# Optimization experiments

Measured on AMD Instinct MI355X. Metric: run time of the kernel, lower is better.

Reference implementation:

```python
import jax, jax.numpy as jnp
import numpy as np

D_STATE = 11
DT_RANK = 4
BN_EPS = 1e-5
RMS_EPS = 1e-5


def setup_inputs() -> dict:
    key = jax.random.key(0)
    ks = jax.random.split(key, 8)
    B, L, D = 8, 8192, 64
    x = jax.random.normal(ks[0], (B, L, D), dtype=jnp.float32)
    tconv_w = jax.random.normal(ks[1], (64, 1, 63), dtype=jnp.float32) * 0.1
    bn_gamma = jnp.ones((64,), jnp.float32)
    bn_beta = jnp.zeros((64,), jnp.float32)
    x_proj_weight = jax.random.normal(ks[2], (1, DT_RANK + 2 * D_STATE, 64), jnp.float32) * (64 ** -0.5)
    dt_projs_weight = jax.random.uniform(ks[3], (1, 64, DT_RANK), jnp.float32, -0.5, 0.5)
    # dt bias ~ inverse-softplus of dt in [1e-3, 1e-1]
    dt = jnp.exp(jax.random.uniform(ks[4], (1, 64), jnp.float32) * (np.log(0.1) - np.log(0.001)) + np.log(0.001))
    dt_projs_bias = dt + jnp.log(-jnp.expm1(-dt))
    A_logs = jnp.log(jnp.broadcast_to(jnp.arange(1, D_STATE + 1, dtype=jnp.float32), (64, D_STATE)))
    Ds = jnp.ones((64,), jnp.float32)
    rms_scale = jnp.ones((1, 64), jnp.float32)
    return {"x": x, "tconv_w": tconv_w, "bn_gamma": bn_gamma, "bn_beta": bn_beta,
            "x_proj_weight": x_proj_weight, "dt_projs_weight": dt_projs_weight,
            "dt_projs_bias": dt_projs_bias, "A_logs": A_logs, "Ds": Ds,
            "rms_scale": rms_scale}


def _silu(v):
    return v * jax.nn.sigmoid(v)


def reference(x, tconv_w, bn_gamma, bn_beta, x_proj_weight, dt_projs_weight,
              dt_projs_bias, A_logs, Ds, rms_scale):
    B, L, D = x.shape  # D == 64
    z = x
    xc = jnp.transpose(x, (0, 2, 1))  # (B, C, L)

    # depthwise conv1d, kernel 63, pad 31, no bias
    xc = jax.lax.conv_general_dilated(
        xc, tconv_w, window_strides=(1,), padding=[(31, 31)],
        feature_group_count=D, dimension_numbers=("NCH", "OIH", "NCH"))

    # BatchNorm1d (training-mode forward: batch stats, biased variance)
    mean = jnp.mean(xc, axis=(0, 2), keepdims=True)
    var = jnp.mean((xc - mean) ** 2, axis=(0, 2), keepdims=True)
    xc = (xc - mean) / jnp.sqrt(var + BN_EPS) * bn_gamma[None, :, None] + bn_beta[None, :, None]

    u = _silu(xc)  # (B, d_inner, L)

    # x_proj: (B,d,L) x (C,d) -> (B,C,L)
    x_dbl = jnp.einsum("bdl,cd->bcl", u, x_proj_weight[0])
    dts = x_dbl[:, :DT_RANK]                      # (B, r, L)
    Bs = x_dbl[:, DT_RANK:DT_RANK + D_STATE]      # (B, N, L)
    Cs = x_dbl[:, DT_RANK + D_STATE:]             # (B, N, L)

    dts = jnp.einsum("brl,dr->bdl", dts, dt_projs_weight[0])
    delta = jax.nn.softplus(dts + dt_projs_bias[0][None, :, None])  # (B,d,L)

    A = -jnp.exp(A_logs)  # (d, N)
    dA = jnp.exp(jnp.einsum("bdl,dn->lbdn", delta, A))      # (L,B,d,N)
    dBu = jnp.einsum("bdl,bnl->lbdn", delta * u, Bs)        # (L,B,d,N)

    def step(h, inp):
        dA_t, dBu_t = inp
        h = dA_t * h + dBu_t
        return h, h

    h0 = jnp.zeros((B, u.shape[1], D_STATE), dtype=u.dtype)
    _, hs = jax.lax.scan(step, h0, (dA, dBu))  # (L,B,d,N)

    y = jnp.einsum("lbdn,bnl->bdl", hs, Cs) + Ds[None, :, None] * u  # (B,d,L)

    y = jnp.transpose(y, (0, 2, 1))  # (B, L, d_inner)

    # RMSNorm
    ms = jnp.mean(y ** 2, axis=-1, keepdims=True)
    y = (rms_scale / jnp.sqrt(ms + RMS_EPS)) * y

    out = y * _silu(z)
    return out
```

## Files before the change

### kernel.cpp

```cpp
#include <hip/hip_runtime.h>
#include <hip/hip_bf16.h>
#include <math.h>

#define NB 8
#define LL 8192
#define DD 64
#define NS 11
#define NR 4
#define NC 512
#define LC (LL/NC)
#define CONV_LT 64
#define KW 63
#define PJ 64
#define NBKT 16
#define US 68
#define WS 72

__device__ __forceinline__ float sigmoidf_(float v){ return 1.f/(1.f+__expf(-v)); }

__global__ void k_zero(float* __restrict__ p){
  p[blockIdx.x*256 + threadIdx.x] = 0.f;
}

__global__ __launch_bounds__(256,4) void k_conv(const float* __restrict__ x,
                                              const float* __restrict__ w,
                                              float* __restrict__ xc,
                                              float* __restrict__ bn_acc){
  const int b  = blockIdx.x / (LL/CONV_LT);
  const int lt = blockIdx.x % (LL/CONV_LT);
  const int l0 = lt*CONV_LT;
  __shared__ float xt[(CONV_LT+62)*DD];
  __shared__ float rs[256], rq[256];
  const int t = threadIdx.x;
  for (int i=t; i<(CONV_LT+62)*DD; i+=256){
    int lrel = i/DD, d = i%DD;
    int lg = l0 - 31 + lrel;
    xt[i] = (lg>=0 && lg<LL) ? x[((size_t)b*LL+lg)*DD + d] : 0.f;
  }
  __syncthreads();
  const int d = t & 63;
  const int base = (t >> 6) * 16;
  float acc[16];
  #pragma unroll
  for (int j=0;j<16;j++) acc[j]=0.f;
  #pragma unroll 1
  for (int kb=0; kb<4; ++kb){
    float wv[16];
    #pragma unroll
    for (int kk=0;kk<16;kk++){
      int k = kb*16+kk;
      wv[kk] = (k<KW) ? w[d*KW+k] : 0.f;
    }
    float xw[31];
    #pragma unroll
    for (int i=0;i<31;i++) xw[i] = xt[(base+kb*16+i)*DD + d];
    #pragma unroll
    for (int j=0;j<16;j++){
      #pragma unroll
      for (int kk=0;kk<16;kk++){
        acc[j] = fmaf(wv[kk], xw[j+kk], acc[j]);
      }
    }
  }
  float lsum=0.f, lsq=0.f;
  #pragma unroll
  for (int j=0;j<16;j++){
    xc[((size_t)b*LL + l0+base+j)*DD + d] = acc[j];
    lsum += acc[j]; lsq = fmaf(acc[j],acc[j],lsq);
  }
  rs[t]=lsum; rq[t]=lsq;
  __syncthreads();
  if (t<64){
    float s = rs[t]+rs[t+64]+rs[t+128]+rs[t+192];
    float q = rq[t]+rq[t+64]+rq[t+128]+rq[t+192];
    const int bkt = (blockIdx.x & (NBKT-1))*128;
    atomicAdd(&bn_acc[bkt+t],    s);
    atomicAdd(&bn_acc[bkt+64+t], q);
  }
}

__global__ __launch_bounds__(256,4) void k_proj(const float* __restrict__ xc,
                                              const float* __restrict__ bn_acc,
                                              const float* __restrict__ gamma,
                                              const float* __restrict__ beta,
                                              const float* __restrict__ xpw,
                                              const float* __restrict__ dtw,
                                              const float* __restrict__ dtb,
                                              const float* __restrict__ Alog,
                                              float* __restrict__ duo,
                                              float* __restrict__ bc,
                                              float* __restrict__ chunkst){
  const int b  = blockIdx.x / (LL/PJ);
  const int lt = blockIdx.x % (LL/PJ);
  const int l0 = lt*PJ;
  __shared__ float ul[PJ*US];
  __shared__ float bcl[PJ][24];
  __shared__ float wsh2[26*WS];
  __shared__ float xd[PJ*NR];
  __shared__ float dtwsh[64*NR];
  const int t = threadIdx.x;
  for (int i=t; i<26*64; i+=256){ int c=i>>6, dd=i&63; wsh2[c*WS+dd] = xpw[i]; }
  dtwsh[t] = dtw[t];
  const int d = t & 63, wv = t >> 6;
  float msum = 0.f, qsum = 0.f;
  #pragma unroll
  for (int k=0;k<NBKT;k++){
    msum += bn_acc[k*128 + d];
    qsum += bn_acc[k*128 + 64 + d];
  }
  const float inv_n = 1.f/((float)NB*(float)LL);
  float mean = msum*inv_n;
  float var  = qsum*inv_n - mean*mean;
  float sc = gamma[d] * rsqrtf(var + 1e-5f);
  float sh = beta[d] - mean*sc;
  float uu[16];
  #pragma unroll
  for (int j=0;j<16;j++){
    int lr = wv*16 + j;
    float v = xc[((size_t)b*LL + l0+lr)*DD + d];
    v = fmaf(v, sc, sh);
    float u_ = v * sigmoidf_(v);
    uu[j] = u_;
    ul[lr*US+d] = u_;
  }
  __syncthreads();
  {
    const int cp  = t & 15;
    const int lrb = t >> 4;
    if (cp < 13){
      float acc0[4] = {0.f,0.f,0.f,0.f};
      float acc1[4] = {0.f,0.f,0.f,0.f};
      #pragma unroll 2
      for (int dd4=0; dd4<16; ++dd4){
        float4 w0 = *reinterpret_cast<const float4*>(&wsh2[(2*cp  )*WS + dd4*4]);
        float4 w1 = *reinterpret_cast<const float4*>(&wsh2[(2*cp+1)*WS + dd4*4]);
        #pragma unroll
        for (int p=0;p<4;p++){
          float4 uv = *reinterpret_cast<const float4*>(&ul[(lrb*4+p)*US + dd4*4]);
          acc0[p] = fmaf(w0.x,uv.x, fmaf(w0.y,uv.y, fmaf(w0.z,uv.z, fmaf(w0.w,uv.w, acc0[p]))));
          acc1[p] = fmaf(w1.x,uv.x, fmaf(w1.y,uv.y, fmaf(w1.z,uv.z, fmaf(w1.w,uv.w, acc1[p]))));
        }
      }
      #pragma unroll
      for (int cc=0; cc<2; ++cc){
        int c = 2*cp+cc;
        #pragma unroll
        for (int p=0;p<4;p++){
          int lr = lrb*4+p;
          float v = cc ? acc1[p] : acc0[p];
          if (c < NR) xd[lr*NR+c] = v;
          else {
            int pos = c - NR;
            int slot = (pos < NS) ? pos : pos+1;
            bcl[lr][slot] = v;
            bc[((size_t)b*LL + l0+lr)*24 + slot] = v;
          }
        }
      }
    }
  }
  __syncthreads();
  {
    const float bias = dtb[d];
    const float dw0 = dtwsh[d*NR+0], dw1 = dtwsh[d*NR+1],
                dw2 = dtwsh[d*NR+2], dw3 = dtwsh[d*NR+3];
    float a0 = -__expf(Alog[d*NS]);
    bool fast = true;
    #pragma unroll
    for (int n=1;n<NS;n++){
      float an = -__expf(Alog[d*NS+n]);
      fast = fast && (fabsf(an - (float)(n+1)*a0) <= 1e-4f*(float)(n+1));
    }
    const int task = b*NC + lt*4 + wv;
    float h[12];
    #pragma unroll
    for (int n=0;n<12;n++) h[n]=0.f;
    float dsum=0.f;
    #pragma unroll 4
    for (int l=0;l<LC;++l){
      int lr = wv*LC + l;
      float4 xv = *reinterpret_cast<const float4*>(&xd[lr*NR]);
      float s = fmaf(dw0,xv.x, fmaf(dw1,xv.y, fmaf(dw2,xv.z, fmaf(dw3,xv.w, bias))));
      float de = fmaxf(s,0.f) + __logf(1.f + __expf(-fabsf(s)));
      float u_ = uu[l];
      float du = de*u_;
      dsum += de;
      float2 st; st.x = de; st.y = u_;
      *reinterpret_cast<float2*>(duo + (((size_t)b*LL + l0+lr)*DD + d)*2) = st;
      float bca[12];
      const float4* q = reinterpret_cast<const float4*>(&bcl[lr][0]);
      *reinterpret_cast<float4*>(&bca[0]) = q[0];
      *reinterpret_cast<float4*>(&bca[4]) = q[1];
      *reinterpret_cast<float4*>(&bca[8]) = q[2];
      if (fast){
        float r = __expf(a0*de);
        float dA = 1.f;
        #pragma unroll
        for (int n=0;n<NS;n++){
          dA *= r;
          h[n] = fmaf(dA, h[n], du*bca[n]);
        }
      } else {
        #pragma unroll
        for (int n=0;n<NS;n++){
          float dA = __expf(-__expf(Alog[d*NS+n])*de);
          h[n] = fmaf(dA, h[n], du*bca[n]);
        }
      }
    }
    h[11] = dsum;
    float4* o = reinterpret_cast<float4*>(chunkst + ((size_t)task*64 + d)*12);
    o[0] = *reinterpret_cast<float4*>(&h[0]);
    o[1] = *reinterpret_cast<float4*>(&h[4]);
    o[2] = *reinterpret_cast<float4*>(&h[8]);
  }
}

__global__ __launch_bounds__(64) void k_scanMid(const float* __restrict__ chunkst,
                                                const float* __restrict__ Alog,
                                                float* __restrict__ hin){
  const int wid  = blockIdx.x;
  const int lane = threadIdx.x & 63;
  const int b = wid >> 6, d = wid & 63;
  const int c0 = lane*8;
  const size_t recbase = (((size_t)b*NC + c0)*64 + d)*12;
  float aAll[NS];
  #pragma unroll
  for (int n=0;n<NS;n++) aAll[n] = -expf(Alog[d*NS+n]);
  bool fast = true;
  #pragma unroll
  for (int n=1;n<NS;n++)
    fast = fast && (fabsf(aAll[n] - (float)(n+1)*aAll[0]) <= 1e-4f*(float)(n+1));
  float Aa[NS], Bb[NS];
  #pragma unroll
  for (int n=0;n<NS;n++){ Aa[n]=1.f; Bb[n]=0.f; }
  #pragma unroll
  for (int j=0;j<8;j++){
    float rec[12];
    const float4* q = reinterpret_cast<const float4*>(chunkst + recbase + (size_t)j*768);
    *reinterpret_cast<float4*>(&rec[0]) = q[0];
    *reinterpret_cast<float4*>(&rec[4]) = q[1];
    *reinterpret_cast<float4*>(&rec[8]) = q[2];
    float ds = rec[11];
    if (fast){
      float r = __expf(aAll[0]*ds);
      float dA = 1.f;
      #pragma unroll
      for (int n=0;n<NS;n++){
        dA *= r;
        Bb[n] = fmaf(dA, Bb[n], rec[n]);
        Aa[n] *= dA;
      }
    } else {
      #pragma unroll
      for (int n=0;n<NS;n++){
        float dA = __expf(aAll[n]*ds);
        Bb[n] = fmaf(dA, Bb[n], rec[n]);
        Aa[n] *= dA;
      }
    }
  }
  #pragma unroll
  for (int n=0;n<NS;n++){
    float A = Aa[n], Bv = Bb[n];
    #pragma unroll
    for (int off=1; off<64; off<<=1){
      float Ap=__shfl_up(A,off,64), Bp=__shfl_up(Bv,off,64);
      if (lane>=off){ Bv = fmaf(A,Bp,Bv); A*=Ap; }
    }
    float hs = __shfl_up(Bv,1,64);
    Bb[n] = (lane==0) ? 0.f : hs;
  }
  #pragma unroll
  for (int j=0;j<8;j++){
    float rec[12];
    const float4* q = reinterpret_cast<const float4*>(chunkst + recbase + (size_t)j*768);
    *reinterpret_cast<float4*>(&rec[0]) = q[0];
    *reinterpret_cast<float4*>(&rec[4]) = q[1];
    *reinterpret_cast<float4*>(&rec[8]) = q[2];
    float ds = rec[11];
    float outv[12];
    if (fast){
      float r = __expf(aAll[0]*ds);
      float dA = 1.f;
      #pragma unroll
      for (int n=0;n<NS;n++){
        outv[n] = Bb[n];
        dA *= r;
        Bb[n] = fmaf(dA, Bb[n], rec[n]);
      }
    } else {
      #pragma unroll
      for (int n=0;n<NS;n++){
        outv[n] = Bb[n];
        float dA = __expf(aAll[n]*ds);
        Bb[n] = fmaf(dA, Bb[n], rec[n]);
      }
    }
    outv[11] = 0.f;
    float4* o = reinterpret_cast<float4*>(hin + recbase + (size_t)j*768);
    o[0] = *reinterpret_cast<float4*>(&outv[0]);
    o[1] = *reinterpret_cast<float4*>(&outv[4]);
    o[2] = *reinterpret_cast<float4*>(&outv[8]);
  }
}

__global__ __launch_bounds__(256,4) void k_scanB(const float* __restrict__ duo,
                                               const float* __restrict__ bc,
                                               const float* __restrict__ Alog,
                                               const float* __restrict__ hin,
                                               const float* __restrict__ Dsv,
                                               const float* __restrict__ rmss,
                                               const float* __restrict__ x,
                                               float* __restrict__ out){
  const int task = blockIdx.x*4 + (threadIdx.x>>6);
  const int d = threadIdx.x & 63;
  const int b = task / NC, c = task % NC;
  float a[NS], h[12];
  #pragma unroll
  for (int n=0;n<NS;n++) a[n] = -expf(Alog[d*NS+n]);
  bool fast = true;
  #pragma unroll
  for (int n=1;n<NS;n++)
    fast = fast && (fabsf(a[n] - (float)(n+1)*a[0]) <= 1e-4f*(float)(n+1));
  {
    const float4* q = reinterpret_cast<const float4*>(hin + ((size_t)task*64 + d)*12);
    *reinterpret_cast<float4*>(&h[0]) = q[0];
    *reinterpret_cast<float4*>(&h[4]) = q[1];
    *reinterpret_cast<float4*>(&h[8]) = q[2];
  }
  const float Dd = Dsv[d];
  const float rsc = rmss[d];
  const int l0 = c*LC;
  #pragma unroll 2
  for (int l=l0; l<l0+LC; ++l){
    size_t p = (size_t)b*LL + l;
    float2 du2 = *reinterpret_cast<const float2*>(duo + (p*DD+d)*2);
    float de = du2.x, uu = du2.y;
    float du = de*uu;
    float bca[24];
    const float4* q = reinterpret_cast<const float4*>(bc + p*24);
    *reinterpret_cast<float4*>(&bca[0])  = q[0];
    *reinterpret_cast<float4*>(&bca[4])  = q[1];
    *reinterpret_cast<float4*>(&bca[8])  = q[2];
    *reinterpret_cast<float4*>(&bca[12]) = q[3];
    *reinterpret_cast<float4*>(&bca[16]) = q[4];
    *reinterpret_cast<float4*>(&bca[20]) = q[5];
    float y = Dd*uu;
    if (fast){
      float r = __expf(a[0]*de);
      float dA = 1.f;
      #pragma unroll
      for (int n=0;n<NS;n++){
        dA *= r;
        h[n] = fmaf(dA, h[n], du*bca[n]);
        y = fmaf(h[n], bca[12+n], y);
      }
    } else {
      #pragma unroll
      for (int n=0;n<NS;n++){
        float dA = __expf(a[n]*de);
        h[n] = fmaf(dA, h[n], du*bca[n]);
        y = fmaf(h[n], bca[12+n], y);
      }
    }
    float ss = y*y;
    #pragma unroll
    for (int m=1;m<64;m<<=1) ss += __shfl_xor(ss, m, 64);
    float yn = rsc * rsqrtf(ss*(1.f/64.f) + 1e-5f) * y;
    float z = x[p*DD+d];
    out[p*DD+d] = yn * (z * sigmoidf_(z));
  }
}

extern "C" void kernel_launch(void* const* d_in, const int* in_sizes, int n_in,
                              void* d_out, int out_size, void* d_ws, size_t ws_size,
                              hipStream_t stream) {
  const float* x     = (const float*)d_in[0];
  const float* w     = (const float*)d_in[1];
  const float* gamma = (const float*)d_in[2];
  const float* beta  = (const float*)d_in[3];
  const float* xpw   = (const float*)d_in[4];
  const float* dtw   = (const float*)d_in[5];
  const float* dtb   = (const float*)d_in[6];
  const float* Alog  = (const float*)d_in[7];
  const float* Dsv   = (const float*)d_in[8];
  const float* rmss  = (const float*)d_in[9];
  float* out = (float*)d_out;

  float* f = (float*)d_ws;
  const size_t n_xld = (size_t)NB*LL*DD;
  float* xc      = f;
  float* duo     = xc + n_xld;
  float* bc      = duo + 2*n_xld;
  float* chunkst = bc + (size_t)NB*LL*24;
  float* hin     = chunkst + (size_t)NB*NC*64*12;
  float* bn_acc  = hin + (size_t)NB*NC*64*12;

  k_zero   <<<NBKT*128/256, 256, 0, stream>>>(bn_acc);
  k_conv   <<<NB*(LL/CONV_LT), 256, 0, stream>>>(x, w, xc, bn_acc);
  k_proj   <<<NB*(LL/PJ), 256, 0, stream>>>(xc, bn_acc, gamma, beta, xpw, dtw, dtb, Alog, duo, bc, chunkst);
  k_scanMid<<<NB*DD, 64, 0, stream>>>(chunkst, Alog, hin);
  k_scanB  <<<(NB*NC)/4, 256, 0, stream>>>(duo, bc, Alog, hin, Dsv, rmss, x, out);
}
```

Baseline: 95.10 us.

## Enlarge conv tiles, spread BN buckets, pack delta/u pairs as float4

The conv kernel now uses 128-row tiles with 512 threads, so fewer halo rows are reloaded per output row. BatchNorm partial sums are spread over 64 atomic buckets to reduce contention, and k_proj reduces those buckets in parallel across its four waves. The delta/u intermediate is stored two timesteps at a time as float4, so the scan kernel does wider loads. The scan kernel also drops its per-lane A array to save registers and recomputes exponentials on the slow path instead.

```diff
diff --git a/kernel.cpp b/kernel.cpp
--- a/kernel.cpp
+++ b/kernel.cpp
@@ -9,10 +9,10 @@
 #define NR 4
 #define NC 512
 #define LC (LL/NC)
-#define CONV_LT 64
+#define CONV_LT 128
 #define KW 63
 #define PJ 64
-#define NBKT 16
+#define NBKT 64
 #define US 68
 #define WS 72
 
@@ -22,7 +22,7 @@
   p[blockIdx.x*256 + threadIdx.x] = 0.f;
 }
 
-__global__ __launch_bounds__(256,4) void k_conv(const float* __restrict__ x,
+__global__ __launch_bounds__(512,4) void k_conv(const float* __restrict__ x,
                                               const float* __restrict__ w,
                                               float* __restrict__ xc,
                                               float* __restrict__ bn_acc){
@@ -30,9 +30,9 @@
   const int lt = blockIdx.x % (LL/CONV_LT);
   const int l0 = lt*CONV_LT;
   __shared__ float xt[(CONV_LT+62)*DD];
-  __shared__ float rs[256], rq[256];
+  __shared__ float rs[512], rq[512];
   const int t = threadIdx.x;
-  for (int i=t; i<(CONV_LT+62)*DD; i+=256){
+  for (int i=t; i<(CONV_LT+62)*DD; i+=512){
     int lrel = i/DD, d = i%DD;
     int lg = l0 - 31 + lrel;
     xt[i] = (lg>=0 && lg<LL) ? x[((size_t)b*LL+lg)*DD + d] : 0.f;
@@ -71,8 +71,9 @@
   rs[t]=lsum; rq[t]=lsq;
   __syncthreads();
   if (t<64){
-    float s = rs[t]+rs[t+64]+rs[t+128]+rs[t+192];
-    float q = rq[t]+rq[t+64]+rq[t+128]+rq[t+192];
+    float s=0.f, q=0.f;
+    #pragma unroll
+    for (int g=0; g<8; ++g){ s += rs[t+64*g]; q += rq[t+64*g]; }
     const int bkt = (blockIdx.x & (NBKT-1))*128;
     atomicAdd(&bn_acc[bkt+t],    s);
     atomicAdd(&bn_acc[bkt+64+t], q);
@@ -98,16 +99,23 @@
   __shared__ float wsh2[26*WS];
   __shared__ float xd[PJ*NR];
   __shared__ float dtwsh[64*NR];
+  __shared__ float bnred[2][4][64];
   const int t = threadIdx.x;
   for (int i=t; i<26*64; i+=256){ int c=i>>6, dd=i&63; wsh2[c*WS+dd] = xpw[i]; }
   dtwsh[t] = dtw[t];
   const int d = t & 63, wv = t >> 6;
-  float msum = 0.f, qsum = 0.f;
-  #pragma unroll
-  for (int k=0;k<NBKT;k++){
-    msum += bn_acc[k*128 + d];
-    qsum += bn_acc[k*128 + 64 + d];
-  }
+  {
+    float ms=0.f, qs=0.f;
+    #pragma unroll
+    for (int k=wv*16; k<wv*16+16; ++k){
+      ms += bn_acc[k*128 + d];
+      qs += bn_acc[k*128 + 64 + d];
+    }
+    bnred[0][wv][d]=ms; bnred[1][wv][d]=qs;
+  }
+  __syncthreads();
+  float msum = bnred[0][0][d]+bnred[0][1][d]+bnred[0][2][d]+bnred[0][3][d];
+  float qsum = bnred[1][0][d]+bnred[1][1][d]+bnred[1][2][d]+bnred[1][3][d];
   const float inv_n = 1.f/((float)NB*(float)LL);
   float mean = msum*inv_n;
   float var  = qsum*inv_n - mean*mean;
@@ -176,6 +184,7 @@
     #pragma unroll
     for (int n=0;n<12;n++) h[n]=0.f;
     float dsum=0.f;
+    float de_prev=0.f, u_prev=0.f;
     #pragma unroll 4
     for (int l=0;l<LC;++l){
       int lr = wv*LC + l;
@@ -185,8 +194,12 @@
       float u_ = uu[l];
       float du = de*u_;
       dsum += de;
-      float2 st; st.x = de; st.y = u_;
-      *reinterpret_cast<float2*>(duo + (((size_t)b*LL + l0+lr)*DD + d)*2) = st;
+      if ((l & 1)==0){ de_prev = de; u_prev = u_; }
+      else {
+        float4 st; st.x = de_prev; st.y = u_prev; st.z = de; st.w = u_;
+        size_t ph = (size_t)b*(LL/2) + (size_t)(l0 + lr - 1)/2;
+        *reinterpret_cast<float4*>(duo + (ph*DD + d)*4) = st;
+      }
       float bca[12];
       const float4* q = reinterpret_cast<const float4*>(&bcl[lr][0]);
       *reinterpret_cast<float4*>(&bca[0]) = q[0];
@@ -316,13 +329,14 @@
   const int task = blockIdx.x*4 + (threadIdx.x>>6);
   const int d = threadIdx.x & 63;
   const int b = task / NC, c = task % NC;
-  float a[NS], h[12];
-  #pragma unroll
-  for (int n=0;n<NS;n++) a[n] = -expf(Alog[d*NS+n]);
+  float a0 = -expf(Alog[d*NS]);
   bool fast = true;
   #pragma unroll
-  for (int n=1;n<NS;n++)
-    fast = fast && (fabsf(a[n] - (float)(n+1)*a[0]) <= 1e-4f*(float)(n+1));
+  for (int n=1;n<NS;n++){
+    float an = -expf(Alog[d*NS+n]);
+    fast = fast && (fabsf(an - (float)(n+1)*a0) <= 1e-4f*(float)(n+1));
+  }
+  float h[12];
   {
     const float4* q = reinterpret_cast<const float4*>(hin + ((size_t)task*64 + d)*12);
     *reinterpret_cast<float4*>(&h[0]) = q[0];
@@ -333,43 +347,48 @@
   const float rsc = rmss[d];
   const int l0 = c*LC;
   #pragma unroll 2
-  for (int l=l0; l<l0+LC; ++l){
-    size_t p = (size_t)b*LL + l;
-    float2 du2 = *reinterpret_cast<const float2*>(duo + (p*DD+d)*2);
-    float de = du2.x, uu = du2.y;
-    float du = de*uu;
-    float bca[24];
-    const float4* q = reinterpret_cast<const float4*>(bc + p*24);
-    *reinterpret_cast<float4*>(&bca[0])  = q[0];
-    *reinterpret_cast<float4*>(&bca[4])  = q[1];
-    *reinterpret_cast<float4*>(&bca[8])  = q[2];
-    *reinterpret_cast<float4*>(&bca[12]) = q[3];
-    *reinterpret_cast<float4*>(&bca[16]) = q[4];
-    *reinterpret_cast<float4*>(&bca[20]) = q[5];
-    float y = Dd*uu;
-    if (fast){
-      float r = __expf(a[0]*de);
-      float dA = 1.f;
-      #pragma unroll
-      for (int n=0;n<NS;n++){
-        dA *= r;
-        h[n] = fmaf(dA, h[n], du*bca[n]);
-        y = fmaf(h[n], bca[12+n], y);
-      }
-    } else {
-      #pragma unroll
-      for (int n=0;n<NS;n++){
-        float dA = __expf(a[n]*de);
-        h[n] = fmaf(dA, h[n], du*bca[n]);
-        y = fmaf(h[n], bca[12+n], y);
-      }
-    }
-    float ss = y*y;
-    #pragma unroll
-    for (int m=1;m<64;m<<=1) ss += __shfl_xor(ss, m, 64);
-    float yn = rsc * rsqrtf(ss*(1.f/64.f) + 1e-5f) * y;
-    float z = x[p*DD+d];
-    out[p*DD+d] = yn * (z * sigmoidf_(z));
+  for (int l2=0; l2<LC; l2+=2){
+    size_t ph = (size_t)b*(LL/2) + (size_t)(l0+l2)/2;
+    float4 dq = *reinterpret_cast<const float4*>(duo + (ph*DD + d)*4);
+    #pragma unroll
+    for (int s=0; s<2; ++s){
+      size_t p = (size_t)b*LL + l0 + l2 + s;
+      float de = s ? dq.z : dq.x;
+      float uu = s ? dq.w : dq.y;
+      float du = de*uu;
+      float bca[24];
+      const float4* q = reinterpret_cast<const float4*>(bc + p*24);
+      *reinterpret_cast<float4*>(&bca[0])  = q[0];
+      *reinterpret_cast<float4*>(&bca[4])  = q[1];
+      *reinterpret_cast<float4*>(&bca[8])  = q[2];
+      *reinterpret_cast<float4*>(&bca[12]) = q[3];
+      *reinterpret_cast<float4*>(&bca[16]) = q[4];
+      *reinterpret_cast<float4*>(&bca[20]) = q[5];
+      float y = Dd*uu;
+      if (fast){
+        float r = __expf(a0*de);
+        float dA = 1.f;
+        #pragma unroll
+        for (int n=0;n<NS;n++){
+          dA *= r;
+          h[n] = fmaf(dA, h[n], du*bca[n]);
+          y = fmaf(h[n], bca[12+n], y);
+        }
+      } else {
+        #pragma unroll
+        for (int n=0;n<NS;n++){
+          float dA = __expf(-expf(Alog[d*NS+n])*de);
+          h[n] = fmaf(dA, h[n], du*bca[n]);
+          y = fmaf(h[n], bca[12+n], y);
+        }
+      }
+      float ss = y*y;
+      #pragma unroll
+      for (int m=1;m<64;m<<=1) ss += __shfl_xor(ss, m, 64);
+      float yn = rsc * rsqrtf(ss*(1.f/64.f) + 1e-5f) * y;
+      float z = x[p*DD+d];
+      out[p*DD+d] = yn * (z * sigmoidf_(z));
+    }
   }
 }
 
@@ -398,7 +417,7 @@
   float* bn_acc  = hin + (size_t)NB*NC*64*12;
 
   k_zero   <<<NBKT*128/256, 256, 0, stream>>>(bn_acc);
-  k_conv   <<<NB*(LL/CONV_LT), 256, 0, stream>>>(x, w, xc, bn_acc);
+  k_conv   <<<NB*(LL/CONV_LT), 512, 0, stream>>>(x, w, xc, bn_acc);
   k_proj   <<<NB*(LL/PJ), 256, 0, stream>>>(xc, bn_acc, gamma, beta, xpw, dtw, dtb, Alog, duo, bc, chunkst);
   k_scanMid<<<NB*DD, 64, 0, stream>>>(chunkst, Alog, hin);
   k_scanB  <<<(NB*NC)/4, 256, 0, stream>>>(duo, bc, Alog, hin, Dsv, rmss, x, out);
```

After: 90.48 us. 1.05x faster.
